# Optimization experiments

Hardware: AMD Instinct MI355X
Metric: run time of the kernel (lower is better)

## Reference

```python
import jax, jax.numpy as jnp
import numpy as np

B, T, C = 2, 2048, 1024
NUM_HEADS = 16
HEAD_DIM = C // NUM_HEADS
TEMP = 1.0
LN_EPS = 1e-6


def setup_inputs() -> dict:
    key = jax.random.key(0)
    kx, kqw, kpw = jax.random.split(key, 3)
    x = jax.random.normal(kx, (B, T, C), dtype=jnp.float32)
    # causal mask, broadcastable to [B, H, T, T]
    mask = jnp.tril(jnp.ones((T, T), dtype=bool))[None, None, :, :]
    # LayerNorm params (flax defaults: scale=1, bias=0)
    ln_scale = jnp.ones((C,), dtype=jnp.float32)
    ln_bias = jnp.zeros((C,), dtype=jnp.float32)
    # xavier_uniform init for dense kernels, zero bias (torch_linear)
    lim_qkv = float(np.sqrt(6.0 / (C + 3 * C)))
    qkv_w = jax.random.uniform(kqw, (C, 3 * C), jnp.float32, -lim_qkv, lim_qkv)
    qkv_b = jnp.zeros((3 * C,), dtype=jnp.float32)
    lim_p = float(np.sqrt(6.0 / (C + C)))
    proj_w = jax.random.uniform(kpw, (C, C), jnp.float32, -lim_p, lim_p)
    proj_b = jnp.zeros((C,), dtype=jnp.float32)
    return {"x": x, "mask": mask, "ln_scale": ln_scale, "ln_bias": ln_bias,
            "qkv_w": qkv_w, "qkv_b": qkv_b, "proj_w": proj_w, "proj_b": proj_b}


def reference(x, mask, ln_scale, ln_bias, qkv_w, qkv_b, proj_w, proj_b):
    b, t, c = x.shape
    # LayerNorm (eps=1e-6, flax default)
    mu = jnp.mean(x, axis=-1, keepdims=True)
    var = jnp.mean(jnp.square(x - mu), axis=-1, keepdims=True)
    xn = (x - mu) * jax.lax.rsqrt(var + LN_EPS) * ln_scale + ln_bias
    # fused QKV projection
    qkv = xn @ qkv_w + qkv_b
    q, k, v = jnp.split(qkv, 3, axis=-1)
    q = q.reshape(b, t, NUM_HEADS, HEAD_DIM) / TEMP
    k = k.reshape(b, t, NUM_HEADS, HEAD_DIM)
    v = v.reshape(b, t, NUM_HEADS, HEAD_DIM)
    # scaled dot-product attention with mask (eval path: no dropout)
    q = q / jnp.sqrt(jnp.float32(HEAD_DIM)).astype(x.dtype)
    scores = jnp.einsum('bqhd,bkhd->bhqk', q, k)  # [B,H,T,T]
    big_neg = jnp.finfo(x.dtype).min
    scores = jnp.where(mask, scores, big_neg)
    attn_weights = jax.nn.softmax(scores, axis=-1).astype(x.dtype)
    out = jnp.einsum('bhqk,bkhd->bqhd', attn_weights, v).reshape(b, t, c)
    return out @ proj_w + proj_b
```

## Files before the change

kernel.cpp:

```cpp
#include <hip/hip_runtime.h>
#include <cstdint>
#include <math.h>

#define DEV __device__ __forceinline__

typedef unsigned int u32;
typedef unsigned short u16;
typedef __attribute__((ext_vector_type(4))) float f32x4;
typedef __attribute__((ext_vector_type(4))) u32 u32x4;
typedef __attribute__((ext_vector_type(2))) u32 u32x2;
typedef __attribute__((ext_vector_type(8))) __bf16 bf16x8;

static_assert(sizeof(bf16x8) == 16, "bf16x8 must be 16B");

static constexpr int Tn = 2048, Cn = 1024;
static constexpr int Mrows = 2 * Tn;
static constexpr float QSCALE2 = 0.125f * 1.44269504088896f;

DEV u16 f2bf_rne(float f) {
  u32 u = __builtin_bit_cast(u32, f);
  u32 r = u + 0x7fffu + ((u >> 16) & 1u);
  return (u16)(r >> 16);
}
DEV float bf2f(u16 h) {
  u32 u = ((u32)h) << 16;
  return __builtin_bit_cast(float, u);
}
DEV u32 pack2bf(float a, float b) {
  return (u32)f2bf_rne(a) | ((u32)f2bf_rne(b) << 16);
}
DEV u32 cvtpk(float lo, float hi) {
  u32 r;
  asm("v_cvt_pk_bf16_f32 %0, %1, %2" : "=v"(r) : "v"(lo), "v"(hi));
  return r;
}
DEV float fexp2(float x) {
#if __has_builtin(__builtin_amdgcn_exp2f)
  return __builtin_amdgcn_exp2f(x);
#else
  return exp2f(x);
#endif
}

DEV void stage16(const void* g, void* l) {
#if __has_builtin(__builtin_amdgcn_global_load_lds)
  __builtin_amdgcn_global_load_lds(
      (__attribute__((address_space(1))) u32*)(uintptr_t)g,
      (__attribute__((address_space(3))) u32*)l, 16, 0, 0);
#else
  *(u32x4*)l = *(const u32x4*)g;
#endif
}

__global__ __launch_bounds__(256) void ln_kernel(const float* __restrict__ x,
                                                 const float* __restrict__ sc,
                                                 const float* __restrict__ bi,
                                                 u16* __restrict__ xn) {
  int row = blockIdx.x;
  int t = threadIdx.x;
  const float* xr = x + (size_t)row * Cn;
  f32x4 v = *(const f32x4*)(xr + t * 4);
  float s = v.x + v.y + v.z + v.w;
  float s2 = v.x * v.x + v.y * v.y + v.z * v.z + v.w * v.w;
#pragma unroll
  for (int off = 1; off < 64; off <<= 1) {
    s += __shfl_xor(s, off);
    s2 += __shfl_xor(s2, off);
  }
  __shared__ float red[8];
  if ((t & 63) == 0) {
    red[(t >> 6) * 2] = s;
    red[(t >> 6) * 2 + 1] = s2;
  }
  __syncthreads();
  s = red[0] + red[2] + red[4] + red[6];
  s2 = red[1] + red[3] + red[5] + red[7];
  float mean = s * (1.0f / Cn);
  float var = s2 * (1.0f / Cn) - mean * mean;
  float rstd = rsqrtf(var + 1e-6f);
  f32x4 g = *(const f32x4*)(sc + t * 4);
  f32x4 b = *(const f32x4*)(bi + t * 4);
  u32 lo = pack2bf((v.x - mean) * rstd * g.x + b.x, (v.y - mean) * rstd * g.y + b.y);
  u32 hi = pack2bf((v.z - mean) * rstd * g.z + b.z, (v.w - mean) * rstd * g.w + b.w);
  u32x2 pack = {lo, hi};
  *(u32x2*)(xn + (size_t)row * Cn + t * 4) = pack;
}

__global__ __launch_bounds__(256) void transpose_cast2(const float* __restrict__ qkv_w,
                                                       u16* __restrict__ wqkv,
                                                       const float* __restrict__ proj_w,
                                                       u16* __restrict__ wproj) {
  __shared__ float tile[32][33];
  int bx = blockIdx.x;
  const float* src;
  u16* dst;
  int Cc;
  if (bx < 96) {
    src = qkv_w; dst = wqkv; Cc = 3072;
  } else {
    src = proj_w; dst = wproj; Cc = 1024; bx -= 96;
  }
  int tx = threadIdx.x, ty = threadIdx.y;
  int c0 = bx * 32, r0 = blockIdx.y * 32;
#pragma unroll
  for (int k = 0; k < 4; ++k)
    tile[ty + 8 * k][tx] = src[(size_t)(r0 + ty + 8 * k) * Cc + c0 + tx];
  __syncthreads();
#pragma unroll
  for (int k = 0; k < 4; ++k)
    dst[(size_t)(c0 + ty + 8 * k) * 1024 + r0 + tx] = f2bf_rne(tile[tx][ty + 8 * k]);
}

__global__ __launch_bounds__(256) void vt_prep(const u16* __restrict__ qkvm,
                                               u16* __restrict__ vt) {
  __shared__ u16 tile[32][33];
  int bh = blockIdx.z;
  int b = bh >> 4, h = bh & 15;
  int t0 = blockIdx.x * 32, d0 = blockIdx.y * 32;
  int tx = threadIdx.x, ty = threadIdx.y;
#pragma unroll
  for (int k = 0; k < 4; ++k)
    tile[ty + 8 * k][tx] =
        qkvm[(size_t)(b * Tn + t0 + ty + 8 * k) * 3072 + 2 * Cn + h * 64 + d0 + tx];
  __syncthreads();
#pragma unroll
  for (int k = 0; k < 4; ++k)
    vt[((size_t)bh * 64 + d0 + ty + 8 * k) * 2048 + t0 + tx] = tile[tx][ty + 8 * k];
}

template <bool OUT_F32, bool QKV_SCALE>
__global__ __launch_bounds__(256, 3) void gemm_kernel(const u16* __restrict__ A,
                                                      const u16* __restrict__ Bt,
                                                      const float* __restrict__ bias,
                                                      void* __restrict__ Cout,
                                                      int Nsz, int Ksz) {
  __shared__ u16 As[128 * 32];
  __shared__ u16 Bs[128 * 32];
  int t = threadIdx.x;
  int l = t & 63, w = t >> 6;
  int quad = l >> 4, c16 = l & 15;
  int wm = w & 1, wn = w >> 1;
  int m0 = blockIdx.y * 128, n0 = blockIdx.x * 128;

  f32x4 acc[4][4];
#pragma unroll
  for (int mt = 0; mt < 4; ++mt)
#pragma unroll
    for (int nt = 0; nt < 4; ++nt) acc[mt][nt] = (f32x4){0.f, 0.f, 0.f, 0.f};

  for (int kk = 0; kk < Ksz; kk += 32) {
#pragma unroll
    for (int i = 0; i < 2; ++i) {
      int c = t + i * 256;
      int m = c >> 2, k8 = (c & 3) ^ ((m >> 1) & 3);
      stage16(A + (size_t)(m0 + m) * Ksz + kk + k8 * 8, (char*)As + c * 16);
    }
#pragma unroll
    for (int i = 0; i < 2; ++i) {
      int c = t + i * 256;
      int n = c >> 2, k8 = (c & 3) ^ ((n >> 1) & 3);
      stage16(Bt + (size_t)(n0 + n) * Ksz + kk + k8 * 8, (char*)Bs + c * 16);
    }
    __syncthreads();
    bf16x8 af[4], bf[4];
#pragma unroll
    for (int mt = 0; mt < 4; ++mt) {
      int m = wm * 64 + mt * 16 + c16;
      int LC = m * 4 + (quad ^ ((m >> 1) & 3));
      af[mt] = *(const bf16x8*)((const char*)As + LC * 16);
    }
#pragma unroll
    for (int nt = 0; nt < 4; ++nt) {
      int n = wn * 64 + nt * 16 + c16;
      int LC = n * 4 + (quad ^ ((n >> 1) & 3));
      bf[nt] = *(const bf16x8*)((const char*)Bs + LC * 16);
    }
#pragma unroll
    for (int mt = 0; mt < 4; ++mt)
#pragma unroll
      for (int nt = 0; nt < 4; ++nt)
        acc[mt][nt] = __builtin_amdgcn_mfma_f32_16x16x32_bf16(af[mt], bf[nt],
                                                              acc[mt][nt], 0, 0, 0);
    __syncthreads();
  }
#pragma unroll
  for (int mt = 0; mt < 4; ++mt) {
    int row = m0 + wm * 64 + mt * 16 + quad * 4;
#pragma unroll
    for (int nt = 0; nt < 4; ++nt) {
      int col = n0 + wn * 64 + nt * 16 + c16;
      float bv = bias[col];
      float scale = (QKV_SCALE && col < 1024) ? QSCALE2 : 1.0f;
#pragma unroll
      for (int r = 0; r < 4; ++r) {
        float v = (acc[mt][nt][r] + bv) * scale;
        if (OUT_F32)
          ((float*)Cout)[(size_t)(row + r) * Nsz + col] = v;
        else
          ((u16*)Cout)[(size_t)(row + r) * Nsz + col] = f2bf_rne(v);
      }
    }
  }
}

__constant__ int4 chunk_tab[31] = {
    {15, 0, 6, 0},  {10, 0, 6, 15}, {5, 0, 6, -1},
    {15, 6, 5, 1},  {15, 11, 5, 2}, {14, 0, 5, 3},  {14, 5, 5, 4},
    {14, 10, 5, 5}, {13, 0, 5, 6},  {13, 5, 5, 7},  {12, 0, 5, 9},
    {10, 6, 5, 16}, {9, 0, 5, 17},  {9, 5, 5, 18},  {8, 0, 5, 19},
    {4, 0, 5, -1},
    {13, 10, 4, 8}, {12, 5, 4, 10}, {12, 9, 4, 11}, {11, 0, 4, 12},
    {11, 4, 4, 13}, {11, 8, 4, 14}, {8, 5, 4, 20},  {7, 0, 4, 21},
    {7, 4, 4, 22},  {6, 0, 4, 23},  {3, 0, 4, -1},
    {6, 4, 3, 24},  {2, 0, 3, -1},
    {1, 0, 2, -1},
    {0, 0, 1, -1}};

__constant__ int2 comb_tab[10] = {{23, 2}, {21, 2}, {19, 2}, {17, 2}, {15, 2},
                                  {12, 3}, {9, 3},  {6, 3},  {3, 3},  {0, 3}};

__global__ __launch_bounds__(256, 2) void flash_kernel(const u16* __restrict__ qkv,
                                                       const u16* __restrict__ vt,
                                                       u16* __restrict__ aout,
                                                       u16* __restrict__ Op,
                                                       float* __restrict__ ml) {
  int4 ck = chunk_tab[blockIdx.x >> 5];
  int bh = blockIdx.x & 31;
  int qt = ck.x, k0 = ck.y, nk = ck.z, slot = ck.w;
  int b = bh >> 4, h = bh & 15;
  int t = threadIdx.x, l = t & 63, w = t >> 6;
  int quad = l >> 4, c16 = l & 15;
  int q0 = qt * 128;

  __shared__ u16 Ks[2][128 * 64];
  __shared__ u16 Ps[128 * 32];

  bf16x8 qf[2][2];
#pragma unroll
  for (int nt = 0; nt < 2; ++nt)
#pragma unroll
    for (int ks = 0; ks < 2; ++ks)
      qf[nt][ks] = *(const bf16x8*)(qkv +
          (size_t)(b * Tn + q0 + w * 32 + nt * 16 + c16) * 3072 +
          h * 64 + ks * 32 + quad * 8);

  const u16* vb[4];
#pragma unroll
  for (int dt = 0; dt < 4; ++dt)
    vb[dt] = vt + ((size_t)bh * 64 + dt * 16 + c16) * 2048 + quad * 8;

  float mrow[2] = {-1e30f, -1e30f};
  float lrow[2] = {0.f, 0.f};
  f32x4 o[2][4];
#pragma unroll
  for (int mq = 0; mq < 2; ++mq)
#pragma unroll
    for (int dt = 0; dt < 4; ++dt) o[mq][dt] = (f32x4){0.f, 0.f, 0.f, 0.f};

#pragma unroll
  for (int i = 0; i < 4; ++i) {
    int c = t + i * 256;
    int key = c >> 3, d8 = (c & 7) ^ (key & 7);
    stage16(qkv + (size_t)(b * Tn + k0 * 128 + key) * 3072 + Cn + h * 64 + d8 * 8,
            (char*)Ks[0] + c * 16);
  }
  __syncthreads();

  for (int it = 0; it < nk; ++it) {
    int kt = k0 + it;
    if (it + 1 < nk) {
#pragma unroll
      for (int i = 0; i < 4; ++i) {
        int c = t + i * 256;
        int key = c >> 3, d8 = (c & 7) ^ (key & 7);
        stage16(qkv + (size_t)(b * Tn + (kt + 1) * 128 + key) * 3072 + Cn +
                    h * 64 + d8 * 8,
                (char*)Ks[(it + 1) & 1] + c * 16);
      }
    }
    const char* Kb = (const char*)Ks[it & 1];

    f32x4 s[8][2];
#pragma unroll
    for (int mt = 0; mt < 8; ++mt)
#pragma unroll
      for (int nt = 0; nt < 2; ++nt) s[mt][nt] = (f32x4){0.f, 0.f, 0.f, 0.f};
#pragma unroll
    for (int mt = 0; mt < 8; ++mt) {
#pragma unroll
      for (int ks = 0; ks < 2; ++ks) {
        int key = mt * 16 + c16;
        int d8 = ks * 4 + quad;
        int LC = key * 8 + (d8 ^ (key & 7));
        bf16x8 kf = *(const bf16x8*)(Kb + LC * 16);
#pragma unroll
        for (int nt = 0; nt < 2; ++nt)
          s[mt][nt] = __builtin_amdgcn_mfma_f32_16x16x32_bf16(kf, qf[nt][ks],
                                                              s[mt][nt], 0, 0, 0);
      }
    }
    if (kt == qt) {
#pragma unroll
      for (int mt = 0; mt < 8; ++mt)
#pragma unroll
        for (int nt = 0; nt < 2; ++nt)
#pragma unroll
          for (int r = 0; r < 4; ++r) {
            int key = kt * 128 + mt * 16 + quad * 4 + r;
            int q = q0 + w * 32 + nt * 16 + c16;
            if (key > q) s[mt][nt][r] = -1e30f;
          }
    }
    float alph[2];
    int needv[2];
#pragma unroll
    for (int nt = 0; nt < 2; ++nt) {
      float m8[8];
#pragma unroll
      for (int mt = 0; mt < 8; ++mt)
        m8[mt] = fmaxf(fmaxf(s[mt][nt][0], s[mt][nt][1]),
                       fmaxf(s[mt][nt][2], s[mt][nt][3]));
      float rm = fmaxf(fmaxf(fmaxf(m8[0], m8[1]), fmaxf(m8[2], m8[3])),
                       fmaxf(fmaxf(m8[4], m8[5]), fmaxf(m8[6], m8[7])));
      rm = fmaxf(rm, __shfl_xor(rm, 16));
      rm = fmaxf(rm, __shfl_xor(rm, 32));
      int need = __any(rm > mrow[nt] + 6.0f);
      needv[nt] = need;
      float mnew = need ? fmaxf(mrow[nt], rm) : mrow[nt];
      alph[nt] = need ? fexp2(mrow[nt] - mnew) : 1.0f;
      mrow[nt] = mnew;
      float part[8];
#pragma unroll
      for (int mt = 0; mt < 8; ++mt) {
        float e0 = fexp2(s[mt][nt][0] - mnew);
        float e1 = fexp2(s[mt][nt][1] - mnew);
        float e2 = fexp2(s[mt][nt][2] - mnew);
        float e3 = fexp2(s[mt][nt][3] - mnew);
        s[mt][nt][0] = e0; s[mt][nt][1] = e1;
        s[mt][nt][2] = e2; s[mt][nt][3] = e3;
        part[mt] = (e0 + e1) + (e2 + e3);
      }
      float rs = ((part[0] + part[1]) + (part[2] + part[3])) +
                 ((part[4] + part[5]) + (part[6] + part[7]));
      rs += __shfl_xor(rs, 16);
      rs += __shfl_xor(rs, 32);
      lrow[nt] = lrow[nt] * alph[nt] + rs;
    }
#pragma unroll
    for (int mq = 0; mq < 2; ++mq)
      if (needv[mq]) {
#pragma unroll
        for (int r = 0; r < 4; ++r) {
          float a = __shfl(alph[mq], quad * 4 + r);
#pragma unroll
          for (int dt = 0; dt < 4; ++dt) o[mq][dt][r] *= a;
        }
      }
#pragma unroll
    for (int ksq = 0; ksq < 4; ++ksq) {
      bf16x8 vf[4];
#pragma unroll
      for (int dt = 0; dt < 4; ++dt)
        vf[dt] = *(const bf16x8*)(vb[dt] + kt * 128 + ksq * 32);
#pragma unroll
      for (int mtp = 0; mtp < 2; ++mtp) {
        int mt = ksq * 2 + mtp;
#pragma unroll
        for (int nt = 0; nt < 2; ++nt) {
          int q = w * 32 + nt * 16 + c16;
          int g = (mtp * 2 + (quad >> 1)) ^ (c16 & 3);
          u32x2 pk = {cvtpk(s[mt][nt][0], s[mt][nt][1]),
                      cvtpk(s[mt][nt][2], s[mt][nt][3])};
          *(u32x2*)((char*)Ps + q * 64 + g * 16 + (quad & 1) * 8) = pk;
        }
      }
      bf16x8 pa[2];
#pragma unroll
      for (int mq = 0; mq < 2; ++mq) {
        int q = w * 32 + mq * 16 + c16;
        pa[mq] = *(const bf16x8*)((const char*)Ps + q * 64 +
                                  ((quad ^ (c16 & 3)) * 16));
      }
#pragma unroll
      for (int dt = 0; dt < 4; ++dt)
#pragma unroll
        for (int mq = 0; mq < 2; ++mq)
          o[mq][dt] = __builtin_amdgcn_mfma_f32_16x16x32_bf16(pa[mq], vf[dt],
                                                              o[mq][dt], 0, 0, 0);
    }
    __syncthreads();
  }

  float linv[2] = {1.0f / lrow[0], 1.0f / lrow[1]};
  if (slot < 0) {
#pragma unroll
    for (int mq = 0; mq < 2; ++mq)
#pragma unroll
      for (int r = 0; r < 4; ++r) {
        float li = __shfl(linv[mq], quad * 4 + r);
        int q = q0 + w * 32 + mq * 16 + quad * 4 + r;
#pragma unroll
        for (int dt = 0; dt < 4; ++dt)
          aout[(size_t)(b * Tn + q) * 1024 + h * 64 + dt * 16 + c16] =
              f2bf_rne(o[mq][dt][r] * li);
      }
  } else {
    int ps = slot * 32 + bh;
#pragma unroll
    for (int mq = 0; mq < 2; ++mq)
#pragma unroll
      for (int r = 0; r < 4; ++r) {
        float li = __shfl(linv[mq], quad * 4 + r);
        int qr = w * 32 + mq * 16 + quad * 4 + r;
#pragma unroll
        for (int dt = 0; dt < 4; ++dt)
          Op[((size_t)ps * 128 + qr) * 64 + dt * 16 + c16] =
              f2bf_rne(o[mq][dt][r] * li);
      }
    if (quad == 0) {
#pragma unroll
      for (int nt = 0; nt < 2; ++nt) {
        int qr = w * 32 + nt * 16 + c16;
        ml[((size_t)ps * 128 + qr) * 2] = mrow[nt];
        ml[((size_t)ps * 128 + qr) * 2 + 1] = lrow[nt];
      }
    }
  }
}

__global__ __launch_bounds__(256) void combine_kernel(const u16* __restrict__ Op,
                                                      const float* __restrict__ ml,
                                                      u16* __restrict__ aout) {
  int qt = 6 + (blockIdx.x >> 5);
  int bh = blockIdx.x & 31;
  int b = bh >> 4, h = bh & 15;
  int2 cb = comb_tab[qt - 6];
  int base = cb.x, n = cb.y;
  int d = threadIdx.x & 63, rq = threadIdx.x >> 6;
  for (int r = 0; r < 32; ++r) {
    int row = rq * 32 + r;
    float mv[3], lv[3], ov[3];
#pragma unroll
    for (int i = 0; i < 3; ++i) {
      int ps = (base + (i < n ? i : 0)) * 32 + bh;
      bool valid = i < n;
      mv[i] = valid ? ml[((size_t)ps * 128 + row) * 2] : -1e30f;
      lv[i] = valid ? ml[((size_t)ps * 128 + row) * 2 + 1] : 0.f;
      ov[i] = valid ? bf2f(Op[((size_t)ps * 128 + row) * 64 + d]) : 0.f;
    }
    float M = fmaxf(fmaxf(mv[0], mv[1]), mv[2]);
    float w0 = fexp2(mv[0] - M) * lv[0];
    float w1 = fexp2(mv[1] - M) * lv[1];
    float w2 = fexp2(mv[2] - M) * lv[2];
    float inv = 1.0f / (w0 + w1 + w2);
    aout[(size_t)(b * Tn + qt * 128 + row) * 1024 + h * 64 + d] =
        f2bf_rne((w0 * ov[0] + w1 * ov[1] + w2 * ov[2]) * inv);
  }
}

extern "C" void kernel_launch(void* const* d_in, const int* in_sizes, int n_in,
                              void* d_out, int out_size, void* d_ws, size_t ws_size,
                              hipStream_t stream) {
  const float* x = (const float*)d_in[0];
  const float* ln_s = (const float*)d_in[2];
  const float* ln_b = (const float*)d_in[3];
  const float* qkv_w = (const float*)d_in[4];
  const float* qkv_b = (const float*)d_in[5];
  const float* proj_w = (const float*)d_in[6];
  const float* proj_b = (const float*)d_in[7];
  float* out = (float*)d_out;
  char* ws = (char*)d_ws;

  u16* xn = (u16*)ws;
  u16* wqkv = (u16*)(ws + (8ull << 20));
  u16* wproj = (u16*)(ws + (14ull << 20));
  u16* qkvm = (u16*)(ws + (16ull << 20));
  u16* attn = (u16*)(ws + (40ull << 20));
  u16* vt = (u16*)(ws + (48ull << 20));
  u16* Op = (u16*)ws;
  float* ml = (float*)(ws + (13ull << 20));

  ln_kernel<<<Mrows, 256, 0, stream>>>(x, ln_s, ln_b, xn);
  transpose_cast2<<<dim3(128, 32), dim3(32, 8), 0, stream>>>(qkv_w, wqkv, proj_w,
                                                             wproj);
  gemm_kernel<false, true><<<dim3(24, 32), 256, 0, stream>>>(xn, wqkv, qkv_b, qkvm,
                                                             3072, 1024);
  vt_prep<<<dim3(64, 2, 32), dim3(32, 8), 0, stream>>>(qkvm, vt);
  flash_kernel<<<992, 256, 0, stream>>>(qkvm, vt, attn, Op, ml);
  combine_kernel<<<320, 256, 0, stream>>>(Op, ml, attn);
  gemm_kernel<true, false><<<dim3(8, 32), 256, 0, stream>>>(attn, wproj, proj_b, out,
                                                            1024, 1024);
}
```

Measured before the change: 249.8 us.

## Stage V tiles into double-buffered LDS alongside K and reswizzle P buffer

The V operand fragments used to be loaded straight from global memory inside the PV loop. They are now staged cooperatively into a double-buffered, XOR-swizzled shared-memory tile in the same prefetch step as K, so they overlap with compute. The P scratch buffer layout is also changed to pair rows and use an 8-way swizzle, which should reduce LDS bank conflicts. This raises shared memory per block by 32 KB, which may limit occupancy at two blocks per CU.

```diff
diff --git a/kernel.cpp b/kernel.cpp
--- a/kernel.cpp
+++ b/kernel.cpp
@@ -233,6 +233,7 @@
   int q0 = qt * 128;
 
   __shared__ u16 Ks[2][128 * 64];
+  __shared__ u16 Vs[2][64 * 128];
   __shared__ u16 Ps[128 * 32];
 
   bf16x8 qf[2][2];
@@ -244,11 +245,6 @@
           (size_t)(b * Tn + q0 + w * 32 + nt * 16 + c16) * 3072 +
           h * 64 + ks * 32 + quad * 8);
 
-  const u16* vb[4];
-#pragma unroll
-  for (int dt = 0; dt < 4; ++dt)
-    vb[dt] = vt + ((size_t)bh * 64 + dt * 16 + c16) * 2048 + quad * 8;
-
   float mrow[2] = {-1e30f, -1e30f};
   float lrow[2] = {0.f, 0.f};
   f32x4 o[2][4];
@@ -257,28 +253,31 @@
 #pragma unroll
     for (int dt = 0; dt < 4; ++dt) o[mq][dt] = (f32x4){0.f, 0.f, 0.f, 0.f};
 
-#pragma unroll
-  for (int i = 0; i < 4; ++i) {
-    int c = t + i * 256;
-    int key = c >> 3, d8 = (c & 7) ^ (key & 7);
-    stage16(qkv + (size_t)(b * Tn + k0 * 128 + key) * 3072 + Cn + h * 64 + d8 * 8,
-            (char*)Ks[0] + c * 16);
-  }
+  auto stageKV = [&](int buf, int kt) {
+#pragma unroll
+    for (int i = 0; i < 4; ++i) {
+      int c = t + i * 256;
+      int key = c >> 3, d8 = (c & 7) ^ (key & 7);
+      stage16(qkv + (size_t)(b * Tn + kt * 128 + key) * 3072 + Cn + h * 64 + d8 * 8,
+              (char*)Ks[buf] + c * 16);
+    }
+#pragma unroll
+    for (int i = 0; i < 4; ++i) {
+      int c = t + i * 256;
+      int d = c >> 4, k8 = (c & 15) ^ (d & 15);
+      stage16(vt + ((size_t)bh * 64 + d) * 2048 + kt * 128 + k8 * 8,
+              (char*)Vs[buf] + c * 16);
+    }
+  };
+
+  stageKV(0, k0);
   __syncthreads();
 
   for (int it = 0; it < nk; ++it) {
     int kt = k0 + it;
-    if (it + 1 < nk) {
-#pragma unroll
-      for (int i = 0; i < 4; ++i) {
-        int c = t + i * 256;
-        int key = c >> 3, d8 = (c & 7) ^ (key & 7);
-        stage16(qkv + (size_t)(b * Tn + (kt + 1) * 128 + key) * 3072 + Cn +
-                    h * 64 + d8 * 8,
-                (char*)Ks[(it + 1) & 1] + c * 16);
-      }
-    }
+    if (it + 1 < nk) stageKV((it + 1) & 1, kt + 1);
     const char* Kb = (const char*)Ks[it & 1];
+    const char* Vb = (const char*)Vs[it & 1];
 
     f32x4 s[8][2];
 #pragma unroll
@@ -358,35 +357,35 @@
       }
 #pragma unroll
     for (int ksq = 0; ksq < 4; ++ksq) {
-      bf16x8 vf[4];
-#pragma unroll
-      for (int dt = 0; dt < 4; ++dt)
-        vf[dt] = *(const bf16x8*)(vb[dt] + kt * 128 + ksq * 32);
 #pragma unroll
       for (int mtp = 0; mtp < 2; ++mtp) {
         int mt = ksq * 2 + mtp;
 #pragma unroll
         for (int nt = 0; nt < 2; ++nt) {
           int q = w * 32 + nt * 16 + c16;
-          int g = (mtp * 2 + (quad >> 1)) ^ (c16 & 3);
+          int ch = ((q & 1) * 4 + mtp * 2 + (quad >> 1)) ^ (c16 & 7);
           u32x2 pk = {cvtpk(s[mt][nt][0], s[mt][nt][1]),
                       cvtpk(s[mt][nt][2], s[mt][nt][3])};
-          *(u32x2*)((char*)Ps + q * 64 + g * 16 + (quad & 1) * 8) = pk;
+          *(u32x2*)((char*)Ps + (q >> 1) * 128 + ch * 16 + (quad & 1) * 8) = pk;
         }
       }
       bf16x8 pa[2];
 #pragma unroll
       for (int mq = 0; mq < 2; ++mq) {
         int q = w * 32 + mq * 16 + c16;
-        pa[mq] = *(const bf16x8*)((const char*)Ps + q * 64 +
-                                  ((quad ^ (c16 & 3)) * 16));
-      }
-#pragma unroll
-      for (int dt = 0; dt < 4; ++dt)
+        int ch = ((q & 1) * 4 + quad) ^ (c16 & 7);
+        pa[mq] = *(const bf16x8*)((const char*)Ps + (q >> 1) * 128 + ch * 16);
+      }
+#pragma unroll
+      for (int dt = 0; dt < 4; ++dt) {
+        int d = dt * 16 + c16;
+        int vc = d * 16 + ((ksq * 4 + quad) ^ (d & 15));
+        bf16x8 vf = *(const bf16x8*)(Vb + vc * 16);
 #pragma unroll
         for (int mq = 0; mq < 2; ++mq)
-          o[mq][dt] = __builtin_amdgcn_mfma_f32_16x16x32_bf16(pa[mq], vf[dt],
+          o[mq][dt] = __builtin_amdgcn_mfma_f32_16x16x32_bf16(pa[mq], vf,
                                                               o[mq][dt], 0, 0, 0);
+      }
     }
     __syncthreads();
   }
```

Measured after the change: 241.2 us. 1.04x faster.
